# Performance work log

Hardware: AMD Instinct MI355X
Metric: run time of the kernel (lower is better)

## Reference

```python
import jax, jax.numpy as jnp
import numpy as np
import math

B, N, D_IN, D_V, H, D_FF = 8, 2048, 256, 256, 8, 512
HD = D_V // H  # head dim = 32
EPS = 1e-5


def layernorm(x, g, b):
    mu = jnp.mean(x, axis=-1, keepdims=True)
    var = jnp.mean(jnp.square(x - mu), axis=-1, keepdims=True)
    return (x - mu) * jax.lax.rsqrt(var + EPS) * g + b


def setup_inputs() -> dict:
    key = jax.random.key(0)
    ks = jax.random.split(key, 12)
    s = 1.0 / math.sqrt(D_IN)
    return {
        "x": jax.random.normal(ks[0], (B, N, D_IN), jnp.float32),
        "y": jax.random.normal(ks[1], (B, N, D_IN), jnp.float32),
        "Wq": jax.random.normal(ks[2], (D_IN, D_V), jnp.float32) * s,
        "bq": jnp.zeros((D_V,), jnp.float32),
        "Wk": jax.random.normal(ks[3], (D_IN, D_V), jnp.float32) * s,
        "bk": jnp.zeros((D_V,), jnp.float32),
        "Wv": jax.random.normal(ks[4], (D_IN, D_V), jnp.float32) * s,
        "bv": jnp.zeros((D_V,), jnp.float32),
        "W1": jax.random.normal(ks[5], (D_V, D_FF), jnp.float32) * s,
        "b1": jnp.zeros((D_FF,), jnp.float32),
        "W2": jax.random.normal(ks[6], (D_FF, D_V), jnp.float32) * (1.0 / math.sqrt(D_FF)),
        "b2": jnp.zeros((D_V,), jnp.float32),
        "ln0_g": jnp.ones((D_IN,), jnp.float32),
        "ln0_b": jnp.zeros((D_IN,), jnp.float32),
        "ln1_g": jnp.ones((D_V,), jnp.float32),
        "ln1_b": jnp.zeros((D_V,), jnp.float32),
    }


def reference(x, y, Wq, bq, Wk, bk, Wv, bv, W1, b1, W2, b2, ln0_g, ln0_b, ln1_g, ln1_b):
    xn = layernorm(x, ln0_g, ln0_b)                      # ln0 on queries
    Q = (xn @ Wq + bq).reshape(B, N, H, HD)              # [B,Nq,H,hd]
    K = (y @ Wk + bk).reshape(B, N, H, HD)
    V = (y @ Wv + bv).reshape(B, N, H, HD)
    # NOTE: faithful scale = 1/sqrt(dim_V) (full model dim), not head dim
    S = jnp.einsum("bqhd,bkhd->bhqk", Q, K) / math.sqrt(D_V)
    A = jax.nn.softmax(S, axis=-1)
    O = Q + jnp.einsum("bhqk,bkhd->bqhd", A, V)          # per-head residual Q_ + A
    O = O.reshape(B, N, D_V)
    On = layernorm(O, ln1_g, ln1_b)
    ff = jax.nn.gelu(On @ W1 + b1, approximate=False) @ W2 + b2
    return O + ff
```

## Files before the change

kernel.cpp:

```cpp
#include <hip/hip_runtime.h>
#include <math.h>

#define RTOT 16384
#define NSEQ 2048
#define NHEAD 8
#define HDIM 32
#define QSCALE 0.09017132252479462f
#define QINV (1.0f / QSCALE)

typedef __attribute__((ext_vector_type(8))) short short8;
typedef __attribute__((ext_vector_type(4))) float f32x4;
typedef __attribute__((ext_vector_type(4))) unsigned uint4v;

#define GLOBAL_AS(p) ((__attribute__((address_space(1))) void*)(p))
#define LDS_AS(p) ((__attribute__((address_space(3))) void*)(p))

__device__ __forceinline__ unsigned pack_bf16(float a, float b) {
  unsigned ua = __float_as_uint(a) + 0x8000u;
  unsigned ub = __float_as_uint(b) + 0x8000u;
  return (ua >> 16) | (ub & 0xffff0000u);
}
__device__ __forceinline__ unsigned pack_bf16_perm(float a, float b) {
  return __builtin_amdgcn_perm(__float_as_uint(b), __float_as_uint(a),
                               0x07060302u);
}
__device__ __forceinline__ ushort bf16_1(float a) {
  return (ushort)((__float_as_uint(a) + 0x8000u) >> 16);
}
__device__ __forceinline__ float bf16_to_f(ushort u) {
  return __uint_as_float(((unsigned)u) << 16);
}
__device__ __forceinline__ short8 frag4(unsigned a0, unsigned a1, unsigned a2,
                                        unsigned a3) {
  uint4v t = {a0, a1, a2, a3};
  return __builtin_bit_cast(short8, t);
}

__global__ __launch_bounds__(256) void stage0_kernel(
    const float* __restrict__ x, const float* __restrict__ y,
    const float* __restrict__ Wq, const float* __restrict__ Wk,
    const float* __restrict__ Wv, const float* __restrict__ W1,
    const float* __restrict__ W2, const float* __restrict__ ln0g,
    const float* __restrict__ ln0b, ushort* __restrict__ Wqt,
    ushort* __restrict__ Wkt, ushort* __restrict__ Wvt,
    ushort* __restrict__ W1t, ushort* __restrict__ W2t,
    ushort* __restrict__ yh, ushort* __restrict__ xh) {
  const int bid = blockIdx.x;
  const int t = threadIdx.x;
  if (bid < 112) {
    const float* W;
    ushort* Wt;
    int K, N, tile;
    if (bid < 16) { W = Wq; Wt = Wqt; K = 256; N = 256; tile = bid; }
    else if (bid < 32) { W = Wk; Wt = Wkt; K = 256; N = 256; tile = bid - 16; }
    else if (bid < 48) { W = Wv; Wt = Wvt; K = 256; N = 256; tile = bid - 32; }
    else if (bid < 80) { W = W1; Wt = W1t; K = 256; N = 512; tile = bid - 48; }
    else { W = W2; Wt = W2t; K = 512; N = 256; tile = bid - 80; }
    const int tn = N >> 6;
    const int k0 = (tile / tn) << 6, n0 = (tile % tn) << 6;
    __shared__ float T[64][65];
#pragma unroll
    for (int i = 0; i < 16; ++i) {
      const int idx = t + i * 256;
      const int r = idx >> 6, c = idx & 63;
      T[r][c] = W[(size_t)(k0 + r) * N + n0 + c];
    }
    __syncthreads();
#pragma unroll
    for (int i = 0; i < 16; ++i) {
      const int idx = t + i * 256;
      const int r = idx >> 6, c = idx & 63;
      Wt[(size_t)(n0 + r) * K + k0 + c] = bf16_1(T[c][r]);
    }
  } else if (bid < 4208) {
    const size_t i = ((size_t)(bid - 112) * 256 + t) * 4;
    const float4 v = *(const float4*)&y[i];
    uint2 pk;
    pk.x = pack_bf16(v.x, v.y);
    pk.y = pack_bf16(v.z, v.w);
    *(uint2*)&yh[i] = pk;
  } else {
    const int lane = t & 63, wave = t >> 6;
    const size_t row = (size_t)(bid - 4208) * 4 + wave;
    const float* xr = x + row * 256;
    float4 v = *(const float4*)&xr[lane * 4];
    float s = v.x + v.y + v.z + v.w;
#pragma unroll
    for (int m = 1; m < 64; m <<= 1) s += __shfl_xor(s, m, 64);
    const float mu = s * (1.0f / 256.0f);
    const float dx = v.x - mu, dy = v.y - mu, dz = v.z - mu, dw = v.w - mu;
    float ss = dx * dx + dy * dy + dz * dz + dw * dw;
#pragma unroll
    for (int m = 1; m < 64; m <<= 1) ss += __shfl_xor(ss, m, 64);
    const float rstd = rsqrtf(ss * (1.0f / 256.0f) + 1e-5f);
    const float4 gv = *(const float4*)&ln0g[lane * 4];
    const float4 bv = *(const float4*)&ln0b[lane * 4];
    uint2 pk;
    pk.x = pack_bf16(dx * rstd * gv.x + bv.x, dy * rstd * gv.y + bv.y);
    pk.y = pack_bf16(dz * rstd * gv.z + bv.z, dw * rstd * gv.w + bv.w);
    *(uint2*)&xh[row * 256 + lane * 4] = pk;
  }
}

__global__ __launch_bounds__(256) void ln_kernel(
    const float* __restrict__ X, const float* __restrict__ g,
    const float* __restrict__ bt, ushort* __restrict__ Yh) {
  const int lane = threadIdx.x & 63;
  const int wave = threadIdx.x >> 6;
  const size_t row = (size_t)blockIdx.x * 4 + wave;
  const float* xr = X + row * 256;
  float4 v = *(const float4*)&xr[lane * 4];
  float s = v.x + v.y + v.z + v.w;
#pragma unroll
  for (int m = 1; m < 64; m <<= 1) s += __shfl_xor(s, m, 64);
  const float mu = s * (1.0f / 256.0f);
  const float dx = v.x - mu, dy = v.y - mu, dz = v.z - mu, dw = v.w - mu;
  float ss = dx * dx + dy * dy + dz * dz + dw * dw;
#pragma unroll
  for (int m = 1; m < 64; m <<= 1) ss += __shfl_xor(ss, m, 64);
  const float rstd = rsqrtf(ss * (1.0f / 256.0f) + 1e-5f);
  const float4 gv = *(const float4*)&g[lane * 4];
  const float4 bv = *(const float4*)&bt[lane * 4];
  uint2 pk;
  pk.x = pack_bf16(dx * rstd * gv.x + bv.x, dy * rstd * gv.y + bv.y);
  pk.y = pack_bf16(dz * rstd * gv.z + bv.z, dw * rstd * gv.w + bv.w);
  *(uint2*)&Yh[row * 256 + lane * 4] = pk;
}

__global__ __launch_bounds__(256) void qkv_kernel(
    const ushort* __restrict__ xh, const ushort* __restrict__ yh,
    const ushort* __restrict__ Wqt, const ushort* __restrict__ Wkt,
    const ushort* __restrict__ Wvt, const float* __restrict__ bq,
    const float* __restrict__ bk, const float* __restrict__ bv,
    ushort* __restrict__ Qh, ushort* __restrict__ Kh,
    ushort* __restrict__ VhT) {
  __shared__ union UU {
    struct { ushort As[2][128 * 32]; ushort Bs[2][2][64 * 32]; } s;
    ushort Ct[64 * 136];
  } u;
  const int t = threadIdx.x;
  const int lane = t & 63, wave = t >> 6;
  const int l16 = lane & 15, quad = lane >> 4;
  const int row0 = blockIdx.x * 128;
  const int ny = blockIdx.y;
  const bool isQ = ny >= 4;
  const int n0 = (ny & 3) << 6;
  const ushort* A = isQ ? xh : yh;
  const int mrow = (wave & 1) * 64, ncol = (wave >> 1) * 32;

  const ushort* gA0 = A + (size_t)(row0 + (t >> 2)) * 256 + ((t & 3) << 3);
  const ushort* gA1 = gA0 + (size_t)64 * 256;
  const ushort* gB0 = (isQ ? Wqt : Wkt) +
                      (size_t)(n0 + (t >> 2)) * 256 + ((t & 3) << 3);
  const ushort* gB1 = Wvt + (size_t)(n0 + (t >> 2)) * 256 + ((t & 3) << 3);

  auto stage = [&](int buf, int kc) {
    __builtin_amdgcn_global_load_lds(GLOBAL_AS(gA0 + kc),
                                     LDS_AS(u.s.As[buf] + 8 * t), 16, 0, 0);
    __builtin_amdgcn_global_load_lds(GLOBAL_AS(gA1 + kc),
                                     LDS_AS(u.s.As[buf] + 2048 + 8 * t), 16, 0,
                                     0);
    __builtin_amdgcn_global_load_lds(GLOBAL_AS(gB0 + kc),
                                     LDS_AS(u.s.Bs[buf][0] + 8 * t), 16, 0, 0);
    if (!isQ)
      __builtin_amdgcn_global_load_lds(GLOBAL_AS(gB1 + kc),
                                       LDS_AS(u.s.Bs[buf][1] + 8 * t), 16, 0,
                                       0);
  };

  f32x4 acc0[4][2] = {};
  f32x4 acc1[4][2] = {};
  stage(0, 0);
  __syncthreads();
  for (int i = 0; i < 8; ++i) {
    const int cur = i & 1;
    if (i < 7) stage(cur ^ 1, (i + 1) * 32);
    short8 af[4], bfr0[2];
#pragma unroll
    for (int mi = 0; mi < 4; ++mi)
      af[mi] =
          *(const short8*)&u.s.As[cur][(mrow + mi * 16 + l16) * 32 + quad * 8];
#pragma unroll
    for (int nj = 0; nj < 2; ++nj)
      bfr0[nj] = *(const short8*)&u.s
                      .Bs[cur][0][(ncol + nj * 16 + l16) * 32 + quad * 8];
#pragma unroll
    for (int mi = 0; mi < 4; ++mi)
#pragma unroll
      for (int nj = 0; nj < 2; ++nj)
        acc0[mi][nj] = __builtin_amdgcn_mfma_f32_16x16x32_bf16(
            af[mi], bfr0[nj], acc0[mi][nj], 0, 0, 0);
    if (!isQ) {
      short8 bfr1[2];
#pragma unroll
      for (int nj = 0; nj < 2; ++nj)
        bfr1[nj] = *(const short8*)&u.s
                        .Bs[cur][1][(ncol + nj * 16 + l16) * 32 + quad * 8];
#pragma unroll
      for (int mi = 0; mi < 4; ++mi)
#pragma unroll
        for (int nj = 0; nj < 2; ++nj)
          acc1[mi][nj] = __builtin_amdgcn_mfma_f32_16x16x32_bf16(
              af[mi], bfr1[nj], acc1[mi][nj], 0, 0, 0);
    }
    __syncthreads();
  }

  if (isQ) {
#pragma unroll
    for (int nj = 0; nj < 2; ++nj) {
      const int n = n0 + ncol + nj * 16 + l16;
      const float bvv = bq[n];
#pragma unroll
      for (int mi = 0; mi < 4; ++mi)
#pragma unroll
        for (int r = 0; r < 4; ++r) {
          const size_t m = (size_t)row0 + mrow + mi * 16 + quad * 4 + r;
          Qh[m * 256 + n] = bf16_1((acc0[mi][nj][r] + bvv) * QSCALE);
        }
    }
  } else {
#pragma unroll
    for (int nj = 0; nj < 2; ++nj) {
      const int n = n0 + ncol + nj * 16 + l16;
      const float bvv = bk[n];
#pragma unroll
      for (int mi = 0; mi < 4; ++mi)
#pragma unroll
        for (int r = 0; r < 4; ++r) {
          const size_t m = (size_t)row0 + mrow + mi * 16 + quad * 4 + r;
          Kh[m * 256 + n] = bf16_1(acc0[mi][nj][r] + bvv);
        }
    }
    __syncthreads();
#pragma unroll
    for (int nj = 0; nj < 2; ++nj) {
      const int nloc = ncol + nj * 16 + l16;
      const float bvv = bv[n0 + nloc];
#pragma unroll
      for (int mi = 0; mi < 4; ++mi)
#pragma unroll
        for (int r = 0; r < 4; ++r)
          u.Ct[nloc * 136 + mrow + mi * 16 + quad * 4 + r] =
              bf16_1(acc1[mi][nj][r] + bvv);
    }
    __syncthreads();
    const int bb = row0 >> 11, ns0 = row0 & 2047;
#pragma unroll
    for (int i = 0; i < 4; ++i) {
      const int c = t + i * 256;
      const int rr = c >> 4, c8 = (c & 15) << 3;
      *(float4*)&VhT[(size_t)(bb * 256 + n0 + rr) * 2048 + ns0 + c8] =
          *(const float4*)&u.Ct[rr * 136 + c8];
    }
  }
}

__global__ __launch_bounds__(256) void mgemm_kernel(
    const ushort* __restrict__ A, const ushort* __restrict__ Wt,
    const float* __restrict__ bias, ushort* __restrict__ Ch, int K, int N) {
  __shared__ ushort As[2][128 * 32];
  __shared__ ushort Bs[2][64 * 32];
  const int t = threadIdx.x;
  const int lane = t & 63, wave = t >> 6;
  const int l16 = lane & 15, quad = lane >> 4;
  const int row0 = blockIdx.x * 128;
  const int n0 = blockIdx.y << 6;
  const int mrow = (wave & 1) * 64, ncol = (wave >> 1) * 32;

  const ushort* gA0 = A + (size_t)(row0 + (t >> 2)) * K + ((t & 3) << 3);
  const ushort* gA1 = gA0 + (size_t)64 * K;
  const ushort* gB = Wt + (size_t)(n0 + (t >> 2)) * K + ((t & 3) << 3);

  auto stage = [&](int buf, int kc) {
    __builtin_amdgcn_global_load_lds(GLOBAL_AS(gA0 + kc),
                                     LDS_AS(As[buf] + 8 * t), 16, 0, 0);
    __builtin_amdgcn_global_load_lds(GLOBAL_AS(gA1 + kc),
                                     LDS_AS(As[buf] + 2048 + 8 * t), 16, 0, 0);
    __builtin_amdgcn_global_load_lds(GLOBAL_AS(gB + kc),
                                     LDS_AS(Bs[buf] + 8 * t), 16, 0, 0);
  };

  f32x4 acc[4][2] = {};
  const int nt = K >> 5;
  stage(0, 0);
  __syncthreads();
  for (int i = 0; i < nt; ++i) {
    const int cur = i & 1;
    if (i < nt - 1) stage(cur ^ 1, (i + 1) * 32);
    short8 af[4], bfr[2];
#pragma unroll
    for (int mi = 0; mi < 4; ++mi)
      af[mi] = *(const short8*)&As[cur][(mrow + mi * 16 + l16) * 32 + quad * 8];
#pragma unroll
    for (int nj = 0; nj < 2; ++nj)
      bfr[nj] =
          *(const short8*)&Bs[cur][(ncol + nj * 16 + l16) * 32 + quad * 8];
#pragma unroll
    for (int mi = 0; mi < 4; ++mi)
#pragma unroll
      for (int nj = 0; nj < 2; ++nj)
        acc[mi][nj] = __builtin_amdgcn_mfma_f32_16x16x32_bf16(
            af[mi], bfr[nj], acc[mi][nj], 0, 0, 0);
    __syncthreads();
  }
#pragma unroll
  for (int nj = 0; nj < 2; ++nj) {
    const int n = n0 + ncol + nj * 16 + l16;
    const float bvv = bias[n];
#pragma unroll
    for (int mi = 0; mi < 4; ++mi) {
#pragma unroll
      for (int r = 0; r < 4; ++r) {
        const size_t m = (size_t)row0 + mrow + mi * 16 + quad * 4 + r;
        float v = acc[mi][nj][r] + bvv;
        v = 0.5f * v * (1.0f + erff(v * 0.70710678118654752f));
        Ch[m * N + n] = bf16_1(v);
      }
    }
  }
}

__global__ __launch_bounds__(256) void mgemm64_kernel(
    const ushort* __restrict__ A, const ushort* __restrict__ Wt,
    const float* __restrict__ bias, const float* __restrict__ res,
    float* __restrict__ Cf, int K, int N) {
  __shared__ ushort As[2][64 * 32];
  __shared__ ushort Bs[2][64 * 32];
  const int t = threadIdx.x;
  const int lane = t & 63, wave = t >> 6;
  const int l16 = lane & 15, quad = lane >> 4;
  const int row0 = blockIdx.x * 64;
  const int n0 = blockIdx.y << 6;
  const int mrow = (wave & 1) * 32, ncol = (wave >> 1) * 32;

  const ushort* gA = A + (size_t)(row0 + (t >> 2)) * K + ((t & 3) << 3);
  const ushort* gB = Wt + (size_t)(n0 + (t >> 2)) * K + ((t & 3) << 3);

  auto stage = [&](int buf, int kc) {
    __builtin_amdgcn_global_load_lds(GLOBAL_AS(gA + kc),
                                     LDS_AS(As[buf] + 8 * t), 16, 0, 0);
    __builtin_amdgcn_global_load_lds(GLOBAL_AS(gB + kc),
                                     LDS_AS(Bs[buf] + 8 * t), 16, 0, 0);
  };

  f32x4 acc[2][2] = {};
  const int nt = K >> 5;
  stage(0, 0);
  __syncthreads();
  for (int i = 0; i < nt; ++i) {
    const int cur = i & 1;
    if (i < nt - 1) stage(cur ^ 1, (i + 1) * 32);
    short8 af[2], bfr[2];
#pragma unroll
    for (int mi = 0; mi < 2; ++mi)
      af[mi] = *(const short8*)&As[cur][(mrow + mi * 16 + l16) * 32 + quad * 8];
#pragma unroll
    for (int nj = 0; nj < 2; ++nj)
      bfr[nj] =
          *(const short8*)&Bs[cur][(ncol + nj * 16 + l16) * 32 + quad * 8];
#pragma unroll
    for (int mi = 0; mi < 2; ++mi)
#pragma unroll
      for (int nj = 0; nj < 2; ++nj)
        acc[mi][nj] = __builtin_amdgcn_mfma_f32_16x16x32_bf16(
            af[mi], bfr[nj], acc[mi][nj], 0, 0, 0);
    __syncthreads();
  }
#pragma unroll
  for (int nj = 0; nj < 2; ++nj) {
    const int n = n0 + ncol + nj * 16 + l16;
    const float bvv = bias[n];
#pragma unroll
    for (int mi = 0; mi < 2; ++mi) {
#pragma unroll
      for (int r = 0; r < 4; ++r) {
        const size_t m = (size_t)row0 + mrow + mi * 16 + quad * 4 + r;
        Cf[m * N + n] = acc[mi][nj][r] + bvv + res[m * N + n];
      }
    }
  }
}

__global__ __launch_bounds__(256) void attn_kernel(
    const ushort* __restrict__ Qh, const ushort* __restrict__ Kh,
    const ushort* __restrict__ VhT, float* __restrict__ O) {
  __shared__ ushort Ks[2][128][40];
  __shared__ ushort Vt[2][32][136];

  const int t = threadIdx.x;
  const int lane = t & 63, wave = t >> 6;
  const int l16 = lane & 15, quad = lane >> 4;
  const int bh = blockIdx.x & 63;
  const int qt = blockIdx.x >> 6;
  const int b = bh >> 3, h = bh & 7;

  const size_t rowQ0 = (size_t)(b * NSEQ + qt * 128 + wave * 32 + l16);
  const short8 qfrag0 = *(const short8*)&Qh[rowQ0 * 256 + h * HDIM + quad * 8];
  const short8 qfrag1 =
      *(const short8*)&Qh[(rowQ0 + 16) * 256 + h * HDIM + quad * 8];
  const short8 ones = {16256, 16256, 16256, 16256,
                       16256, 16256, 16256, 16256};
  const f32x4 zf = {0.f, 0.f, 0.f, 0.f};

  f32x4 o00 = zf, o01 = zf, o10 = zf, o11 = zf;
  f32x4 s0 = zf, s1 = zf;

  const int kr = t >> 2, kc8 = (t & 3) << 3;
  const int krL = (kr & ~12) | ((kr & 4) << 1) | ((kr & 8) >> 1);
  const int vd = t >> 3, vc8 = (t & 7) << 3;
  const ushort* gK = Kh + ((size_t)(b * NSEQ + krL)) * 256 + h * HDIM + kc8;
  const ushort* gK2 = gK + (size_t)64 * 256;
  const ushort* gV = VhT + ((size_t)(bh * 32 + vd)) * 2048 + vc8;

  float4 kreg0 = *(const float4*)gK;
  float4 kreg1 = *(const float4*)gK2;
  float4 vreg0 = *(const float4*)gV;
  float4 vreg1 = *(const float4*)(gV + 64);

  for (int kt = 0; kt < 16; ++kt) {
    const int bf = kt & 1;
    *(float4*)&Ks[bf][kr][kc8] = kreg0;
    *(float4*)&Ks[bf][64 + kr][kc8] = kreg1;
    *(float4*)&Vt[bf][vd][vc8] = vreg0;
    *(float4*)&Vt[bf][vd][64 + vc8] = vreg1;
    __syncthreads();
    if (kt < 15) {
      const size_t ko = (size_t)(kt + 1) * 128 * 256;
      kreg0 = *(const float4*)(gK + ko);
      kreg1 = *(const float4*)(gK2 + ko);
      vreg0 = *(const float4*)(gV + (kt + 1) * 128);
      vreg1 = *(const float4*)(gV + (kt + 1) * 128 + 64);
    }

#pragma unroll
    for (int half = 0; half < 2; ++half) {
      const int r0 = half * 64;
      const int c0 = half * 64;

      short8 kf[4];
#pragma unroll
      for (int sub = 0; sub < 4; ++sub)
        kf[sub] = *(const short8*)&Ks[bf][r0 + sub * 16 + l16][quad * 8];
      const short8 vf00 = *(const short8*)&Vt[bf][l16][c0 + quad * 8];
      const short8 vf01 = *(const short8*)&Vt[bf][l16][c0 + 32 + quad * 8];
      const short8 vf10 = *(const short8*)&Vt[bf][16 + l16][c0 + quad * 8];
      const short8 vf11 = *(const short8*)&Vt[bf][16 + l16][c0 + 32 + quad * 8];

      f32x4 sa0[4], sa1[4];
#pragma unroll
      for (int sub = 0; sub < 4; ++sub)
        sa0[sub] = __builtin_amdgcn_mfma_f32_16x16x32_bf16(kf[sub], qfrag0, zf,
                                                           0, 0, 0);
#pragma unroll
      for (int sub = 0; sub < 4; ++sub)
        sa1[sub] = __builtin_amdgcn_mfma_f32_16x16x32_bf16(kf[sub], qfrag1, zf,
                                                           0, 0, 0);

      unsigned p0[4][2], p1[4][2];
#pragma unroll
      for (int sub = 0; sub < 4; ++sub) {
        p0[sub][0] = pack_bf16_perm(__builtin_amdgcn_exp2f(sa0[sub][0]),
                                    __builtin_amdgcn_exp2f(sa0[sub][1]));
        p0[sub][1] = pack_bf16_perm(__builtin_amdgcn_exp2f(sa0[sub][2]),
                                    __builtin_amdgcn_exp2f(sa0[sub][3]));
      }
#pragma unroll
      for (int sub = 0; sub < 4; ++sub) {
        p1[sub][0] = pack_bf16_perm(__builtin_amdgcn_exp2f(sa1[sub][0]),
                                    __builtin_amdgcn_exp2f(sa1[sub][1]));
        p1[sub][1] = pack_bf16_perm(__builtin_amdgcn_exp2f(sa1[sub][2]),
                                    __builtin_amdgcn_exp2f(sa1[sub][3]));
      }
      unsigned u00 = p0[0][0], w00 = p0[1][0];
      asm("v_permlane32_swap_b32 %0, %1" : "+v"(u00), "+v"(w00));
      unsigned u01 = p0[0][1], w01 = p0[1][1];
      asm("v_permlane32_swap_b32 %0, %1" : "+v"(u01), "+v"(w01));
      unsigned u02 = p0[2][0], w02 = p0[3][0];
      asm("v_permlane32_swap_b32 %0, %1" : "+v"(u02), "+v"(w02));
      unsigned u03 = p0[2][1], w03 = p0[3][1];
      asm("v_permlane32_swap_b32 %0, %1" : "+v"(u03), "+v"(w03));
      const short8 pf00 = frag4(u00, u01, w00, w01);
      const short8 pf01 = frag4(u02, u03, w02, w03);

      unsigned u10 = p1[0][0], w10 = p1[1][0];
      asm("v_permlane32_swap_b32 %0, %1" : "+v"(u10), "+v"(w10));
      unsigned u11 = p1[0][1], w11 = p1[1][1];
      asm("v_permlane32_swap_b32 %0, %1" : "+v"(u11), "+v"(w11));
      unsigned u12 = p1[2][0], w12 = p1[3][0];
      asm("v_permlane32_swap_b32 %0, %1" : "+v"(u12), "+v"(w12));
      unsigned u13 = p1[2][1], w13 = p1[3][1];
      asm("v_permlane32_swap_b32 %0, %1" : "+v"(u13), "+v"(w13));
      const short8 pf10 = frag4(u10, u11, w10, w11);
      const short8 pf11 = frag4(u12, u13, w12, w13);

      __builtin_amdgcn_s_setprio(1);
      o00 = __builtin_amdgcn_mfma_f32_16x16x32_bf16(pf00, vf00, o00, 0, 0, 0);
      o00 = __builtin_amdgcn_mfma_f32_16x16x32_bf16(pf01, vf01, o00, 0, 0, 0);
      o01 = __builtin_amdgcn_mfma_f32_16x16x32_bf16(pf00, vf10, o01, 0, 0, 0);
      o01 = __builtin_amdgcn_mfma_f32_16x16x32_bf16(pf01, vf11, o01, 0, 0, 0);
      o10 = __builtin_amdgcn_mfma_f32_16x16x32_bf16(pf10, vf00, o10, 0, 0, 0);
      o10 = __builtin_amdgcn_mfma_f32_16x16x32_bf16(pf11, vf01, o10, 0, 0, 0);
      o11 = __builtin_amdgcn_mfma_f32_16x16x32_bf16(pf10, vf10, o11, 0, 0, 0);
      o11 = __builtin_amdgcn_mfma_f32_16x16x32_bf16(pf11, vf11, o11, 0, 0, 0);
      s0 = __builtin_amdgcn_mfma_f32_16x16x32_bf16(pf00, ones, s0, 0, 0, 0);
      s0 = __builtin_amdgcn_mfma_f32_16x16x32_bf16(pf01, ones, s0, 0, 0, 0);
      s1 = __builtin_amdgcn_mfma_f32_16x16x32_bf16(pf10, ones, s1, 0, 0, 0);
      s1 = __builtin_amdgcn_mfma_f32_16x16x32_bf16(pf11, ones, s1, 0, 0, 0);
      __builtin_amdgcn_s_setprio(0);
    }
  }

#pragma unroll
  for (int g = 0; g < 2; ++g) {
    const f32x4 oS = g ? s1 : s0;
    const f32x4 oa = g ? o10 : o00;
    const f32x4 ob = g ? o11 : o01;
    const size_t row0 =
        (size_t)(b * NSEQ + qt * 128 + wave * 32 + g * 16 + quad * 4);
#pragma unroll
    for (int r = 0; r < 4; ++r) {
      const float il = 1.0f / oS[r];
      const size_t ro = (row0 + r) * 256 + h * HDIM + l16;
      O[ro] = bf16_to_f(Qh[ro]) * QINV + oa[r] * il;
      O[ro + 16] = bf16_to_f(Qh[ro + 16]) * QINV + ob[r] * il;
    }
  }
}

extern "C" void kernel_launch(void* const* d_in, const int* in_sizes, int n_in,
                              void* d_out, int out_size, void* d_ws, size_t ws_size,
                              hipStream_t stream) {
  const float* x = (const float*)d_in[0];
  const float* y = (const float*)d_in[1];
  const float* Wq = (const float*)d_in[2];
  const float* bq = (const float*)d_in[3];
  const float* Wk = (const float*)d_in[4];
  const float* bk = (const float*)d_in[5];
  const float* Wv = (const float*)d_in[6];
  const float* bv = (const float*)d_in[7];
  const float* W1 = (const float*)d_in[8];
  const float* b1 = (const float*)d_in[9];
  const float* W2 = (const float*)d_in[10];
  const float* b2 = (const float*)d_in[11];
  const float* ln0g = (const float*)d_in[12];
  const float* ln0b = (const float*)d_in[13];
  const float* ln1g = (const float*)d_in[14];
  const float* ln1b = (const float*)d_in[15];
  float* out = (float*)d_out;
  char* base = (char*)d_ws;

  const size_t RM = (size_t)RTOT * 256;
  ushort* yh = (ushort*)base;
  float* Ob = (float*)base;
  ushort* Qh = (ushort*)(base + 2 * RM * 4);
  ushort* Kh = (ushort*)(base + 2 * RM * 4 + RM * 2);
  ushort* VhT = (ushort*)(base + 3 * RM * 4);
  ushort* xh = (ushort*)(base + 3 * RM * 4 + RM * 2);
  ushort* Onh = xh;
  ushort* Hidh = Qh;
  char* wbase = base + 4 * RM * 4;
  ushort* Wqt = (ushort*)wbase;
  ushort* Wkt = Wqt + 65536;
  ushort* Wvt = Wkt + 65536;
  ushort* W1t = Wvt + 65536;
  ushort* W2t = W1t + 131072;

  stage0_kernel<<<8304, 256, 0, stream>>>(x, y, Wq, Wk, Wv, W1, W2, ln0g, ln0b,
                                          Wqt, Wkt, Wvt, W1t, W2t, yh, xh);
  qkv_kernel<<<dim3(128, 8), 256, 0, stream>>>(xh, yh, Wqt, Wkt, Wvt, bq, bk,
                                               bv, Qh, Kh, VhT);
  attn_kernel<<<1024, 256, 0, stream>>>(Qh, Kh, VhT, Ob);
  ln_kernel<<<RTOT / 4, 256, 0, stream>>>(Ob, ln1g, ln1b, Onh);
  mgemm_kernel<<<dim3(128, 8), 256, 0, stream>>>(Onh, W1t, b1, Hidh, 256, 512);
  mgemm64_kernel<<<dim3(256, 4), 256, 0, stream>>>(Hidh, W2t, b2, Ob, out, 512,
                                                   256);
}
```

Measured before the change: 212.0 us.

## Fuse post-attention LayerNorm into the first FFN GEMM kernel

Removes the standalone ln_kernel and folds LayerNorm of the attention output into the W1 GEMM. Each block normalizes 32 rows into LDS as bf16 and runs the GEMM against a 128-wide column tile of W1, with GELU in the epilogue. This saves one launch and a bf16 round trip through global memory. In exchange, each row is re-normalized by all 4 column blocks, the M tile shrinks from 128 to 32 rows (less A reuse per W1 load), and the fp32 input is read four times.

New measurement: 216.8 us. 2.2% more time.

```diff
diff --git a/kernel.cpp b/kernel.cpp
--- a/kernel.cpp
+++ b/kernel.cpp
@@ -102,31 +102,6 @@
   }
 }
 
-__global__ __launch_bounds__(256) void ln_kernel(
-    const float* __restrict__ X, const float* __restrict__ g,
-    const float* __restrict__ bt, ushort* __restrict__ Yh) {
-  const int lane = threadIdx.x & 63;
-  const int wave = threadIdx.x >> 6;
-  const size_t row = (size_t)blockIdx.x * 4 + wave;
-  const float* xr = X + row * 256;
-  float4 v = *(const float4*)&xr[lane * 4];
-  float s = v.x + v.y + v.z + v.w;
-#pragma unroll
-  for (int m = 1; m < 64; m <<= 1) s += __shfl_xor(s, m, 64);
-  const float mu = s * (1.0f / 256.0f);
-  const float dx = v.x - mu, dy = v.y - mu, dz = v.z - mu, dw = v.w - mu;
-  float ss = dx * dx + dy * dy + dz * dz + dw * dw;
-#pragma unroll
-  for (int m = 1; m < 64; m <<= 1) ss += __shfl_xor(ss, m, 64);
-  const float rstd = rsqrtf(ss * (1.0f / 256.0f) + 1e-5f);
-  const float4 gv = *(const float4*)&g[lane * 4];
-  const float4 bv = *(const float4*)&bt[lane * 4];
-  uint2 pk;
-  pk.x = pack_bf16(dx * rstd * gv.x + bv.x, dy * rstd * gv.y + bv.y);
-  pk.y = pack_bf16(dz * rstd * gv.z + bv.z, dw * rstd * gv.w + bv.w);
-  *(uint2*)&Yh[row * 256 + lane * 4] = pk;
-}
-
 __global__ __launch_bounds__(256) void qkv_kernel(
     const ushort* __restrict__ xh, const ushort* __restrict__ yh,
     const ushort* __restrict__ Wqt, const ushort* __restrict__ Wkt,
@@ -256,67 +231,79 @@
   }
 }
 
-__global__ __launch_bounds__(256) void mgemm_kernel(
-    const ushort* __restrict__ A, const ushort* __restrict__ Wt,
-    const float* __restrict__ bias, ushort* __restrict__ Ch, int K, int N) {
-  __shared__ ushort As[2][128 * 32];
-  __shared__ ushort Bs[2][64 * 32];
+__global__ __launch_bounds__(256) void lnffn1_kernel(
+    const float* __restrict__ Ob, const float* __restrict__ g,
+    const float* __restrict__ bt, const ushort* __restrict__ W1t,
+    const float* __restrict__ b1, ushort* __restrict__ Hidh) {
+  __shared__ ushort Al[32][264];
+  __shared__ ushort Bs[2][128 * 32];
   const int t = threadIdx.x;
   const int lane = t & 63, wave = t >> 6;
   const int l16 = lane & 15, quad = lane >> 4;
-  const int row0 = blockIdx.x * 128;
-  const int n0 = blockIdx.y << 6;
-  const int mrow = (wave & 1) * 64, ncol = (wave >> 1) * 32;
-
-  const ushort* gA0 = A + (size_t)(row0 + (t >> 2)) * K + ((t & 3) << 3);
-  const ushort* gA1 = gA0 + (size_t)64 * K;
-  const ushort* gB = Wt + (size_t)(n0 + (t >> 2)) * K + ((t & 3) << 3);
-
-  auto stage = [&](int buf, int kc) {
-    __builtin_amdgcn_global_load_lds(GLOBAL_AS(gA0 + kc),
-                                     LDS_AS(As[buf] + 8 * t), 16, 0, 0);
-    __builtin_amdgcn_global_load_lds(GLOBAL_AS(gA1 + kc),
-                                     LDS_AS(As[buf] + 2048 + 8 * t), 16, 0, 0);
-    __builtin_amdgcn_global_load_lds(GLOBAL_AS(gB + kc),
+  const size_t row0 = (size_t)blockIdx.x * 32;
+  const int n0 = blockIdx.y << 7;
+  const int mrow = (wave & 1) * 16, ncol = (wave >> 1) * 64;
+
+  const ushort* gB0 = W1t + (size_t)(n0 + (t >> 2)) * 256 + ((t & 3) << 3);
+  const ushort* gB1 = gB0 + (size_t)64 * 256;
+  auto stageB = [&](int buf, int kc) {
+    __builtin_amdgcn_global_load_lds(GLOBAL_AS(gB0 + kc),
                                      LDS_AS(Bs[buf] + 8 * t), 16, 0, 0);
+    __builtin_amdgcn_global_load_lds(GLOBAL_AS(gB1 + kc),
+                                     LDS_AS(Bs[buf] + 2048 + 8 * t), 16, 0, 0);
   };
 
-  f32x4 acc[4][2] = {};
-  const int nt = K >> 5;
-  stage(0, 0);
+  stageB(0, 0);
+
+  const float4 gv = *(const float4*)&g[lane * 4];
+  const float4 bv = *(const float4*)&bt[lane * 4];
+#pragma unroll
+  for (int i = 0; i < 8; ++i) {
+    const int r = i * 4 + wave;
+    const float* xr = Ob + (row0 + r) * 256;
+    float4 v = *(const float4*)&xr[lane * 4];
+    float s = v.x + v.y + v.z + v.w;
+#pragma unroll
+    for (int m = 1; m < 64; m <<= 1) s += __shfl_xor(s, m, 64);
+    const float mu = s * (1.0f / 256.0f);
+    const float dx = v.x - mu, dy = v.y - mu, dz = v.z - mu, dw = v.w - mu;
+    float ss = dx * dx + dy * dy + dz * dz + dw * dw;
+#pragma unroll
+    for (int m = 1; m < 64; m <<= 1) ss += __shfl_xor(ss, m, 64);
+    const float rstd = rsqrtf(ss * (1.0f / 256.0f) + 1e-5f);
+    uint2 pk;
+    pk.x = pack_bf16(dx * rstd * gv.x + bv.x, dy * rstd * gv.y + bv.y);
+    pk.y = pack_bf16(dz * rstd * gv.z + bv.z, dw * rstd * gv.w + bv.w);
+    *(uint2*)&Al[r][lane * 4] = pk;
+  }
   __syncthreads();
-  for (int i = 0; i < nt; ++i) {
+
+  f32x4 acc[4] = {};
+  for (int i = 0; i < 8; ++i) {
     const int cur = i & 1;
-    if (i < nt - 1) stage(cur ^ 1, (i + 1) * 32);
-    short8 af[4], bfr[2];
-#pragma unroll
-    for (int mi = 0; mi < 4; ++mi)
-      af[mi] = *(const short8*)&As[cur][(mrow + mi * 16 + l16) * 32 + quad * 8];
-#pragma unroll
-    for (int nj = 0; nj < 2; ++nj)
-      bfr[nj] =
+    if (i < 7) stageB(cur ^ 1, (i + 1) * 32);
+    const short8 af =
+        *(const short8*)&Al[mrow + l16][i * 32 + quad * 8];
+#pragma unroll
+    for (int nj = 0; nj < 4; ++nj) {
+      const short8 bf =
           *(const short8*)&Bs[cur][(ncol + nj * 16 + l16) * 32 + quad * 8];
-#pragma unroll
-    for (int mi = 0; mi < 4; ++mi)
-#pragma unroll
-      for (int nj = 0; nj < 2; ++nj)
-        acc[mi][nj] = __builtin_amdgcn_mfma_f32_16x16x32_bf16(
-            af[mi], bfr[nj], acc[mi][nj], 0, 0, 0);
-    __syncthreads();
-  }
-#pragma unroll
-  for (int nj = 0; nj < 2; ++nj) {
+      acc[nj] =
+          __builtin_amdgcn_mfma_f32_16x16x32_bf16(af, bf, acc[nj], 0, 0, 0);
+    }
+    __syncthreads();
+  }
+
+#pragma unroll
+  for (int nj = 0; nj < 4; ++nj) {
     const int n = n0 + ncol + nj * 16 + l16;
-    const float bvv = bias[n];
-#pragma unroll
-    for (int mi = 0; mi < 4; ++mi) {
-#pragma unroll
-      for (int r = 0; r < 4; ++r) {
-        const size_t m = (size_t)row0 + mrow + mi * 16 + quad * 4 + r;
-        float v = acc[mi][nj][r] + bvv;
-        v = 0.5f * v * (1.0f + erff(v * 0.70710678118654752f));
-        Ch[m * N + n] = bf16_1(v);
-      }
+    const float bvv = b1[n];
+#pragma unroll
+    for (int r = 0; r < 4; ++r) {
+      const size_t m = row0 + mrow + quad * 4 + r;
+      float v = acc[nj][r] + bvv;
+      v = 0.5f * v * (1.0f + erff(v * 0.70710678118654752f));
+      Hidh[m * 512 + n] = bf16_1(v);
     }
   }
 }
@@ -557,7 +544,6 @@
   ushort* Kh = (ushort*)(base + 2 * RM * 4 + RM * 2);
   ushort* VhT = (ushort*)(base + 3 * RM * 4);
   ushort* xh = (ushort*)(base + 3 * RM * 4 + RM * 2);
-  ushort* Onh = xh;
   ushort* Hidh = Qh;
   char* wbase = base + 4 * RM * 4;
   ushort* Wqt = (ushort*)wbase;
@@ -571,8 +557,8 @@
   qkv_kernel<<<dim3(128, 8), 256, 0, stream>>>(xh, yh, Wqt, Wkt, Wvt, bq, bk,
                                                bv, Qh, Kh, VhT);
   attn_kernel<<<1024, 256, 0, stream>>>(Qh, Kh, VhT, Ob);
-  ln_kernel<<<RTOT / 4, 256, 0, stream>>>(Ob, ln1g, ln1b, Onh);
-  mgemm_kernel<<<dim3(128, 8), 256, 0, stream>>>(Onh, W1t, b1, Hidh, 256, 512);
+  lnffn1_kernel<<<dim3(512, 4), 256, 0, stream>>>(Ob, ln1g, ln1b, W1t, b1,
+                                                  Hidh);
   mgemm64_kernel<<<dim3(256, 4), 256, 0, stream>>>(Hidh, W2t, b2, Ob, out, 512,
                                                    256);
 }
```
